# Kernel optimization log

Hardware: AMD Instinct MI355X
Metric: run time of the kernel (lower is better)

The kernel has to match this reference:

```python
import jax, jax.numpy as jnp
import numpy as np


def setup_inputs() -> dict:
    key = jax.random.key(0)
    ks = jax.random.split(key, 7)
    B, T, I, H, O = 64, 2048, 32, 256, 32
    s = 0.05
    return {
        "x": jax.random.normal(ks[0], (B, T, I), dtype=jnp.float32),
        "W_ih": jax.random.normal(ks[1], (4 * H, I), dtype=jnp.float32) * s,
        "W_hh": jax.random.normal(ks[2], (4 * H, H), dtype=jnp.float32) * s,
        "b_ih": jax.random.normal(ks[3], (4 * H,), dtype=jnp.float32) * s,
        "b_hh": jax.random.normal(ks[4], (4 * H,), dtype=jnp.float32) * s,
        "fc_w": jax.random.normal(ks[5], (O, H), dtype=jnp.float32) * s,
        "fc_b": jax.random.normal(ks[6], (O,), dtype=jnp.float32) * s,
    }


def _lstm(x, W_ih, W_hh, b_ih, b_hh):
    # x: [B,T,I]; PyTorch gate order: i, f, g, o stacked along 4H axis.
    B = x.shape[0]
    H = W_hh.shape[1]
    # Precompute input contributions for all timesteps in one GEMM: [B,T,4H]
    xg = jnp.einsum('bti,gi->btg', x, W_ih) + b_ih + b_hh

    def step(carry, xg_t):
        h, c = carry  # [B,H] each
        gates = xg_t + h @ W_hh.T  # [B,4H]
        i, f, g, o = jnp.split(gates, 4, axis=-1)
        i = jax.nn.sigmoid(i)
        f = jax.nn.sigmoid(f)
        g = jnp.tanh(g)
        o = jax.nn.sigmoid(o)
        c = f * c + i * g
        h = o * jnp.tanh(c)
        return (h, c), h

    h0 = jnp.zeros((B, H), dtype=x.dtype)
    (_, _), hs = jax.lax.scan(step, (h0, h0), jnp.swapaxes(xg, 0, 1))
    return jnp.swapaxes(hs, 0, 1)  # [B,T,H]


def reference(x, W_ih, W_hh, b_ih, b_hh, fc_w, fc_b):
    out = _lstm(x, W_ih, W_hh, b_ih, b_hh)          # [B,T,H]
    # Conv1d(H, O, kernel_size=1) over channel dim == pointwise linear.
    return jnp.einsum('bth,oh->bto', out, fc_w) + fc_b  # [B,T,O]
```

## Files before the change

### kernel.cpp

```cpp
#include <hip/hip_runtime.h>
#include <cstdint>


#define B_  64
#define T_  2048
#define I_  32
#define H_  256
#define O_  32

typedef unsigned int v4u __attribute__((ext_vector_type(4)));
typedef _Float16 h2_t __attribute__((ext_vector_type(2)));

#if __has_builtin(__builtin_amdgcn_sdot4)
__device__ __forceinline__ int dot4(int a, int b, int c) {
    return __builtin_amdgcn_sdot4(a, b, c, false);
}
#else
__device__ __forceinline__ int dot4(int a, int b, int c) {
    c += (int)(int8_t)(a)        * (int)(int8_t)(b);
    c += (int)(int8_t)(a >> 8)   * (int)(int8_t)(b >> 8);
    c += (int)(int8_t)(a >> 16)  * (int)(int8_t)(b >> 16);
    c += (int)(int8_t)(a >> 24)  * (int)(int8_t)(b >> 24);
    return c;
}
#endif

__device__ __forceinline__ float fdot2h(h2_t a, h2_t b, float c) {
#if __has_builtin(__builtin_amdgcn_fdot2)
    return __builtin_amdgcn_fdot2(a, b, c, false);
#else
    return c + (float)a[0] * (float)b[0] + (float)a[1] * (float)b[1];
#endif
}

__device__ __forceinline__ float wave64_max_bcast(float v) {
    int t;
    t = __builtin_amdgcn_update_dpp(__float_as_int(v), __float_as_int(v), 0x111, 0xf, 0xf, false);
    v = fmaxf(v, __int_as_float(t));
    t = __builtin_amdgcn_update_dpp(__float_as_int(v), __float_as_int(v), 0x112, 0xf, 0xf, false);
    v = fmaxf(v, __int_as_float(t));
    t = __builtin_amdgcn_update_dpp(__float_as_int(v), __float_as_int(v), 0x114, 0xf, 0xf, false);
    v = fmaxf(v, __int_as_float(t));
    t = __builtin_amdgcn_update_dpp(__float_as_int(v), __float_as_int(v), 0x118, 0xf, 0xf, false);
    v = fmaxf(v, __int_as_float(t));
    t = __builtin_amdgcn_update_dpp(__float_as_int(v), __float_as_int(v), 0x142, 0xa, 0xf, false);
    v = fmaxf(v, __int_as_float(t));
    t = __builtin_amdgcn_update_dpp(__float_as_int(v), __float_as_int(v), 0x143, 0xc, 0xf, false);
    v = fmaxf(v, __int_as_float(t));
    return __int_as_float(__builtin_amdgcn_readlane(__float_as_int(v), 63));
}

__device__ __forceinline__ float sum8(float v) {
    int t;
    t = __builtin_amdgcn_update_dpp(0, __float_as_int(v), 0x111, 0xf, 0xf, true); v += __int_as_float(t);
    t = __builtin_amdgcn_update_dpp(0, __float_as_int(v), 0x112, 0xf, 0xf, true); v += __int_as_float(t);
    t = __builtin_amdgcn_update_dpp(0, __float_as_int(v), 0x114, 0xf, 0xf, true); v += __int_as_float(t);
    return v;
}

#define QW_OFF   0
#define WIH_OFF  262144
#define S1_OFF   327680
#define BIAS_OFF 331776
#define XH_OFF   335872

__device__ __forceinline__ uint32_t pack_q(int q0, int q1, int q2, int q3) {
    return  ((uint32_t)(uint8_t)(int8_t)q0)
          | (((uint32_t)(uint8_t)(int8_t)q1) << 8)
          | (((uint32_t)(uint8_t)(int8_t)q2) << 16)
          | (((uint32_t)(uint8_t)(int8_t)q3) << 24);
}

__device__ __forceinline__ int clamp127(int v) {
    return v < -127 ? -127 : (v > 127 ? 127 : v);
}

__global__ __launch_bounds__(64) void prep_w(
    const float* __restrict__ Whh, const float* __restrict__ Wih,
    const float* __restrict__ bih, const float* __restrict__ bhh,
    uint32_t* __restrict__ qw4, uint32_t* __restrict__ wih4,
    float* __restrict__ s1v, float* __restrict__ biasv)
{
    const int gr = blockIdx.x;
    const int c  = threadIdx.x;
    const int j  = gr >> 8;
    const int r  = gr & 255;

    const float4 wv = ((const float4*)(Whh + gr * H_))[c];
    float m = fmaxf(fmaxf(fabsf(wv.x), fabsf(wv.y)), fmaxf(fabsf(wv.z), fabsf(wv.w)));
    #pragma unroll
    for (int s = 1; s < 64; s <<= 1) m = fmaxf(m, __shfl_xor(m, s, 64));
    const float S1 = fmaxf(m, 1e-20f) / 127.f;
    const float r1 = 1.f / S1;

    {
        const int d = j * 64 + c;
        qw4[(d >> 2) * 1024 + r * 4 + (d & 3)] = pack_q(
            clamp127((int)rintf(wv.x * r1)), clamp127((int)rintf(wv.y * r1)),
            clamp127((int)rintf(wv.z * r1)), clamp127((int)rintf(wv.w * r1)));
    }
    if (c < 16) {
        union { uint32_t u; h2_t h; } z;
        z.h[0] = (_Float16)Wih[gr * I_ + 2 * c];
        z.h[1] = (_Float16)Wih[gr * I_ + 2 * c + 1];
        const int dd = j * 16 + c;
        wih4[(dd >> 2) * 1024 + r * 4 + (dd & 3)] = z.u;
    }
    if (c == 0) { s1v[gr] = S1; biasv[gr] = bih[gr] + bhh[gr]; }
}

__global__ __launch_bounds__(256) void prep_xh(
    const float* __restrict__ x, uint32_t* __restrict__ xh)
{
    const int i = blockIdx.x * 256 + threadIdx.x;
    const float2 v = ((const float2*)x)[i];
    union { uint32_t u; h2_t h; } z;
    z.h[0] = (_Float16)v.x; z.h[1] = (_Float16)v.y;
    xh[i] = z.u;
}

__global__ __launch_bounds__(256, 1) void lstm_main(
    const uint32_t* __restrict__ qw4, const uint32_t* __restrict__ wih4,
    const float* __restrict__ s1v, const float* __restrict__ biasv,
    const uint32_t* __restrict__ xh, const float* __restrict__ fcw,
    const float* __restrict__ fcb, float* __restrict__ out)
{
    const int b  = blockIdx.x;
    const int r  = threadIdx.x;
    const int ln = r & 63;
    const int wv = r >> 6;

    __shared__ uint32_t hqb[2][64];
    __shared__ __align__(16) float hscb[2][4];
    __shared__ uint32_t hfb[2][128];

    v4u w4[64];
    #pragma unroll
    for (int d4 = 0; d4 < 64; d4++) w4[d4] = ((const v4u*)qw4)[d4 * 256 + r];
    v4u wx[16];
    #pragma unroll
    for (int d4 = 0; d4 < 16; d4++) wx[d4] = ((const v4u*)wih4)[d4 * 256 + r];
    float S1j[4], bj[4];
    #pragma unroll
    for (int j = 0; j < 4; j++) { S1j[j] = s1v[j * 256 + r]; bj[j] = biasv[j * 256 + r]; }

    const int o_ = r >> 3, ks = r & 7;
    h2_t fw[16];
    {
        const float* fr = fcw + o_ * H_ + ks * 32;
        #pragma unroll
        for (int i = 0; i < 16; i++) {
            h2_t p; p[0] = (_Float16)fr[2 * i]; p[1] = (_Float16)fr[2 * i + 1];
            fw[i] = p;
        }
    }
    const float fcb_v = fcb[o_];

    if (r < 4) hscb[1][r] = 0.f;
    __syncthreads();

    const uint32_t* xb   = xh + (size_t)(b * T_) * 16;
    float*          outb = out + (size_t)(b * T_) * O_;

    float c_state = 0.f;

    for (int t = 0; t < T_; t++) {
        const int pb = (t & 1) ^ 1, cb = t & 1;

        const v4u* xv = (const v4u*)(xb + (size_t)t * 16);
        const v4u x0 = xv[0], x1 = xv[1], x2 = xv[2], x3 = xv[3];

        const v4u*   hqv = (const v4u*)&hqb[pb][0];
        const float4 scv = *(const float4*)&hscb[pb][0];
        const float  scar[4] = { scv.x, scv.y, scv.z, scv.w };

        float a0 = 0.f, a1 = 0.f, a2 = 0.f, a3 = 0.f;
        #pragma unroll
        for (int g = 0; g < 4; g++) {
            v4u hg[4];
            #pragma unroll
            for (int q = 0; q < 4; q++) hg[q] = hqv[g * 4 + q];
            int i0 = 0, i1 = 0, i2 = 0, i3 = 0;
            #pragma unroll
            for (int q = 0; q < 4; q++) {
                #pragma unroll
                for (int e = 0; e < 4; e++) {
                    const int hv = (int)hg[q][e];
                    i0 = dot4((int)w4[ 0 + g * 4 + q][e], hv, i0);
                    i1 = dot4((int)w4[16 + g * 4 + q][e], hv, i1);
                    i2 = dot4((int)w4[32 + g * 4 + q][e], hv, i2);
                    i3 = dot4((int)w4[48 + g * 4 + q][e], hv, i3);
                }
            }
            a0 = fmaf((float)i0, scar[g], a0);
            a1 = fmaf((float)i1, scar[g], a1);
            a2 = fmaf((float)i2, scar[g], a2);
            a3 = fmaf((float)i3, scar[g], a3);
        }

        if (t > 0) {
            const v4u* hfv = (const v4u*)&hfb[pb][0];
            v4u fh[4];
            #pragma unroll
            for (int i = 0; i < 4; i++) fh[i] = hfv[ks * 4 + i];
            float acc = 0.f;
            #pragma unroll
            for (int i = 0; i < 16; i++) {
                union { uint32_t u; h2_t h; } z;
                z.u = fh[i >> 2][i & 3];
                acc = fdot2h(fw[i], z.h, acc);
            }
            acc = sum8(acc);
            if (ks == 7) outb[(t - 1) * O_ + o_] = acc + fcb_v;
        }

        float xd0 = 0.f, xd1 = 0.f, xd2 = 0.f, xd3 = 0.f;
        {
            const v4u xg4[4] = { x0, x1, x2, x3 };
            #pragma unroll
            for (int d4 = 0; d4 < 4; d4++) {
                #pragma unroll
                for (int e = 0; e < 4; e++) {
                    union { uint32_t u; h2_t h; } zx, z0, z1, z2, z3;
                    zx.u = xg4[d4][e];
                    z0.u = wx[ 0 + d4][e]; xd0 = fdot2h(z0.h, zx.h, xd0);
                    z1.u = wx[ 4 + d4][e]; xd1 = fdot2h(z1.h, zx.h, xd1);
                    z2.u = wx[ 8 + d4][e]; xd2 = fdot2h(z2.h, zx.h, xd2);
                    z3.u = wx[12 + d4][e]; xd3 = fdot2h(z3.h, zx.h, xd3);
                }
            }
        }

        const float g0 = fmaf(a0, S1j[0], xd0 + bj[0]);
        const float g1 = fmaf(a1, S1j[1], xd1 + bj[1]);
        const float g2 = fmaf(a2, S1j[2], xd2 + bj[2]);
        const float g3 = fmaf(a3, S1j[3], xd3 + bj[3]);
        const float i_ = 1.f / (1.f + __expf(-g0));
        const float f_ = 1.f / (1.f + __expf(-g1));
        const float gg = 2.f / (1.f + __expf(-2.f * g2)) - 1.f;
        const float oo = 1.f / (1.f + __expf(-g3));
        c_state = f_ * c_state + i_ * gg;
        const float tc = 2.f / (1.f + __expf(-2.f * c_state)) - 1.f;
        const float hval = oo * tc;

        float m = wave64_max_bcast(fabsf(hval));
        m = fmaxf(m, 1e-12f);
        const int q = clamp127((int)rintf(hval * (127.f / m)));
        ((char*)&hqb[cb][0])[r] = (char)(int8_t)q;
        if (ln == 0) hscb[cb][wv] = m * (1.f / 127.f);
        ((_Float16*)&hfb[cb][0])[r] = (_Float16)hval;

        asm volatile("s_waitcnt lgkmcnt(0)" ::: "memory");
        __builtin_amdgcn_s_barrier();
    }

    {
        const int pb = (T_ - 1) & 1;
        const v4u* hfv = (const v4u*)&hfb[pb][0];
        v4u fh[4];
        #pragma unroll
        for (int i = 0; i < 4; i++) fh[i] = hfv[ks * 4 + i];
        float acc = 0.f;
        #pragma unroll
        for (int i = 0; i < 16; i++) {
            union { uint32_t u; h2_t h; } z;
            z.u = fh[i >> 2][i & 3];
            acc = fdot2h(fw[i], z.h, acc);
        }
        acc = sum8(acc);
        if (ks == 7) outb[(T_ - 1) * O_ + o_] = acc + fcb_v;
    }
}

extern "C" void kernel_launch(void* const* d_in, const int* in_sizes, int n_in,
                              void* d_out, int out_size, void* d_ws, size_t ws_size,
                              hipStream_t stream) {
    const float* x    = (const float*)d_in[0];
    const float* Wih  = (const float*)d_in[1];
    const float* Whh  = (const float*)d_in[2];
    const float* bih  = (const float*)d_in[3];
    const float* bhh  = (const float*)d_in[4];
    const float* fcw  = (const float*)d_in[5];
    const float* fcb  = (const float*)d_in[6];
    float* out = (float*)d_out;

    char* ws = (char*)d_ws;
    uint32_t* qw4   = (uint32_t*)(ws + QW_OFF);
    uint32_t* wih4  = (uint32_t*)(ws + WIH_OFF);
    float*    s1v   = (float*)(ws + S1_OFF);
    float*    biasv = (float*)(ws + BIAS_OFF);
    uint32_t* xh    = (uint32_t*)(ws + XH_OFF);

    prep_w<<<1024, 64, 0, stream>>>(Whh, Wih, bih, bhh, qw4, wih4, s1v, biasv);
    prep_xh<<<(B_ * T_ * 16) / 256, 256, 0, stream>>>(x, xh);
    lstm_main<<<B_, 256, 0, stream>>>(qw4, wih4, s1v, biasv, xh, fcw, fcb, out);
}
```

Before: 3.410 ms.

## Batch four sequences per block and use MFMA for recurrent, input and FC GEMMs

Replaces the per-sequence dot4 LSTM kernel (64 blocks of 256 threads) with 16 blocks of 512 threads, each processing 4 batch rows at once. The recurrent int8 matmul, the fp16 input projection and the output linear layer now run as MFMA instructions, and the weights are pre-swizzled into MFMA fragment layouts by the prep kernels. Hidden-state quantization now uses a per-batch-row max via LDS atomicMax, which adds a second barrier per timestep. This cuts the number of serial blocks and the scalar dot work per step, at the cost of extra synchronization, padding in the MFMA M dimension, and fewer CUs in use.

```diff
diff --git a/kernel.cpp b/kernel.cpp
--- a/kernel.cpp
+++ b/kernel.cpp
@@ -7,33 +7,18 @@
 #define I_  32
 #define H_  256
 #define O_  32
-
+#define MB  4
+#define NBLK 16
+
+typedef int v4i __attribute__((ext_vector_type(4)));
 typedef unsigned int v4u __attribute__((ext_vector_type(4)));
+typedef float f32x4 __attribute__((ext_vector_type(4)));
+typedef _Float16 f16x8 __attribute__((ext_vector_type(8)));
 typedef _Float16 h2_t __attribute__((ext_vector_type(2)));
 
-#if __has_builtin(__builtin_amdgcn_sdot4)
-__device__ __forceinline__ int dot4(int a, int b, int c) {
-    return __builtin_amdgcn_sdot4(a, b, c, false);
-}
-#else
-__device__ __forceinline__ int dot4(int a, int b, int c) {
-    c += (int)(int8_t)(a)        * (int)(int8_t)(b);
-    c += (int)(int8_t)(a >> 8)   * (int)(int8_t)(b >> 8);
-    c += (int)(int8_t)(a >> 16)  * (int)(int8_t)(b >> 16);
-    c += (int)(int8_t)(a >> 24)  * (int)(int8_t)(b >> 24);
-    return c;
-}
-#endif
-
-__device__ __forceinline__ float fdot2h(h2_t a, h2_t b, float c) {
-#if __has_builtin(__builtin_amdgcn_fdot2)
-    return __builtin_amdgcn_fdot2(a, b, c, false);
-#else
-    return c + (float)a[0] * (float)b[0] + (float)a[1] * (float)b[1];
-#endif
-}
-
-__device__ __forceinline__ float wave64_max_bcast(float v) {
+union U16x8 { v4u u; f16x8 h; };
+
+__device__ __forceinline__ float row16_max(float v) {
     int t;
     t = __builtin_amdgcn_update_dpp(__float_as_int(v), __float_as_int(v), 0x111, 0xf, 0xf, false);
     v = fmaxf(v, __int_as_float(t));
@@ -43,26 +28,15 @@
     v = fmaxf(v, __int_as_float(t));
     t = __builtin_amdgcn_update_dpp(__float_as_int(v), __float_as_int(v), 0x118, 0xf, 0xf, false);
     v = fmaxf(v, __int_as_float(t));
-    t = __builtin_amdgcn_update_dpp(__float_as_int(v), __float_as_int(v), 0x142, 0xa, 0xf, false);
-    v = fmaxf(v, __int_as_float(t));
-    t = __builtin_amdgcn_update_dpp(__float_as_int(v), __float_as_int(v), 0x143, 0xc, 0xf, false);
-    v = fmaxf(v, __int_as_float(t));
-    return __int_as_float(__builtin_amdgcn_readlane(__float_as_int(v), 63));
-}
-
-__device__ __forceinline__ float sum8(float v) {
-    int t;
-    t = __builtin_amdgcn_update_dpp(0, __float_as_int(v), 0x111, 0xf, 0xf, true); v += __int_as_float(t);
-    t = __builtin_amdgcn_update_dpp(0, __float_as_int(v), 0x112, 0xf, 0xf, true); v += __int_as_float(t);
-    t = __builtin_amdgcn_update_dpp(0, __float_as_int(v), 0x114, 0xf, 0xf, true); v += __int_as_float(t);
     return v;
 }
 
-#define QW_OFF   0
-#define WIH_OFF  262144
-#define S1_OFF   327680
-#define BIAS_OFF 331776
-#define XH_OFF   335872
+#define WQ_OFF    0
+#define S1P_OFF   262144
+#define BIASP_OFF 266240
+#define WIHH2_OFF 270336
+#define FCF_OFF   335872
+#define XH_OFF    352256
 
 __device__ __forceinline__ uint32_t pack_q(int q0, int q1, int q2, int q3) {
     return  ((uint32_t)(uint8_t)(int8_t)q0)
@@ -75,38 +49,36 @@
     return v < -127 ? -127 : (v > 127 ? 127 : v);
 }
 
-__global__ __launch_bounds__(64) void prep_w(
+
+__global__ __launch_bounds__(64) void prep_wq(
     const float* __restrict__ Whh, const float* __restrict__ Wih,
     const float* __restrict__ bih, const float* __restrict__ bhh,
-    uint32_t* __restrict__ qw4, uint32_t* __restrict__ wih4,
-    float* __restrict__ s1v, float* __restrict__ biasv)
+    uint32_t* __restrict__ wq2, float* __restrict__ s1p,
+    float* __restrict__ biasp, uint32_t* __restrict__ wihh2)
 {
     const int gr = blockIdx.x;
-    const int c  = threadIdx.x;
-    const int j  = gr >> 8;
-    const int r  = gr & 255;
-
-    const float4 wv = ((const float4*)(Whh + gr * H_))[c];
+    const int j  = threadIdx.x;
+    const int g  = gr >> 8, r = gr & 255;
+    const int c  = ((r >> 4) << 6) | (g << 4) | (r & 15);
+
+    const float4 wv = ((const float4*)(Whh + gr * H_))[j];
     float m = fmaxf(fmaxf(fabsf(wv.x), fabsf(wv.y)), fmaxf(fabsf(wv.z), fabsf(wv.w)));
     #pragma unroll
     for (int s = 1; s < 64; s <<= 1) m = fmaxf(m, __shfl_xor(m, s, 64));
     const float S1 = fmaxf(m, 1e-20f) / 127.f;
     const float r1 = 1.f / S1;
 
-    {
-        const int d = j * 64 + c;
-        qw4[(d >> 2) * 1024 + r * 4 + (d & 3)] = pack_q(
-            clamp127((int)rintf(wv.x * r1)), clamp127((int)rintf(wv.y * r1)),
-            clamp127((int)rintf(wv.z * r1)), clamp127((int)rintf(wv.w * r1)));
-    }
-    if (c < 16) {
+    wq2[((c >> 4) * 16 + (j >> 2)) * 64 + (c & 15) * 4 + (j & 3)] = pack_q(
+        clamp127((int)rintf(wv.x * r1)), clamp127((int)rintf(wv.y * r1)),
+        clamp127((int)rintf(wv.z * r1)), clamp127((int)rintf(wv.w * r1)));
+
+    if (j < 16) {
         union { uint32_t u; h2_t h; } z;
-        z.h[0] = (_Float16)Wih[gr * I_ + 2 * c];
-        z.h[1] = (_Float16)Wih[gr * I_ + 2 * c + 1];
-        const int dd = j * 16 + c;
-        wih4[(dd >> 2) * 1024 + r * 4 + (dd & 3)] = z.u;
-    }
-    if (c == 0) { s1v[gr] = S1; biasv[gr] = bih[gr] + bhh[gr]; }
+        z.h[0] = (_Float16)Wih[gr * I_ + 2 * j];
+        z.h[1] = (_Float16)Wih[gr * I_ + 2 * j + 1];
+        wihh2[((c >> 4) * 4 + (j >> 2)) * 64 + (c & 15) * 4 + (j & 3)] = z.u;
+    }
+    if (j == 0) { s1p[c] = S1; biasp[c] = bih[gr] + bhh[gr]; }
 }
 
 __global__ __launch_bounds__(256) void prep_xh(
@@ -119,156 +91,172 @@
     xh[i] = z.u;
 }
 
-__global__ __launch_bounds__(256, 1) void lstm_main(
-    const uint32_t* __restrict__ qw4, const uint32_t* __restrict__ wih4,
-    const float* __restrict__ s1v, const float* __restrict__ biasv,
-    const uint32_t* __restrict__ xh, const float* __restrict__ fcw,
+__global__ __launch_bounds__(64) void prep_fcf(
+    const float* __restrict__ fcw, uint32_t* __restrict__ fcf)
+{
+    const int id = blockIdx.x * 64 + threadIdx.x;
+    const int fw = id >> 9, rem = id & 511;
+    const int ks = rem >> 6, l = rem & 63;
+    const int o  = fw * 16 + (l & 15);
+    const int kb = ks * 32 + (l >> 4) * 8;
+    const float* src = fcw + o * H_ + kb;
+    #pragma unroll
+    for (int e = 0; e < 4; e++) {
+        union { uint32_t u; h2_t h; } z;
+        z.h[0] = (_Float16)src[2 * e];
+        z.h[1] = (_Float16)src[2 * e + 1];
+        fcf[id * 4 + e] = z.u;
+    }
+}
+
+__global__ __launch_bounds__(512, 2) void lstm_mfma(
+    const uint32_t* __restrict__ wq2, const float* __restrict__ s1p,
+    const float* __restrict__ biasp, const uint32_t* __restrict__ wihh2,
+    const uint32_t* __restrict__ xh, const uint32_t* __restrict__ fcf,
     const float* __restrict__ fcb, float* __restrict__ out)
 {
-    const int b  = blockIdx.x;
-    const int r  = threadIdx.x;
-    const int ln = r & 63;
-    const int wv = r >> 6;
-
-    __shared__ uint32_t hqb[2][64];
-    __shared__ __align__(16) float hscb[2][4];
-    __shared__ uint32_t hfb[2][128];
-
-    v4u w4[64];
+    const int blk = blockIdx.x, tid = threadIdx.x;
+    const int wvi = tid >> 6, l = tid & 63, lq = l >> 4, lo = l & 15;
+    const int b   = lo >> 2;
+
+    __shared__ __align__(16) char     Ab[2][1088];
+    __shared__ __align__(16) _Float16 hf[2][1088];
+    __shared__ int shmax[2][4];
+
+    v4i  wB[8][4];
+    float s1c[8], biasc[8];
     #pragma unroll
-    for (int d4 = 0; d4 < 64; d4++) w4[d4] = ((const v4u*)qw4)[d4 * 256 + r];
-    v4u wx[16];
-    #pragma unroll
-    for (int d4 = 0; d4 < 16; d4++) wx[d4] = ((const v4u*)wih4)[d4 * 256 + r];
-    float S1j[4], bj[4];
-    #pragma unroll
-    for (int j = 0; j < 4; j++) { S1j[j] = s1v[j * 256 + r]; bj[j] = biasv[j * 256 + r]; }
-
-    const int o_ = r >> 3, ks = r & 7;
-    h2_t fw[16];
-    {
-        const float* fr = fcw + o_ * H_ + ks * 32;
+    for (int nt = 0; nt < 8; nt++) {
+        const int c = wvi * 128 + nt * 16 + lo;
+        s1c[nt] = s1p[c]; biasc[nt] = biasp[c];
         #pragma unroll
-        for (int i = 0; i < 16; i++) {
-            h2_t p; p[0] = (_Float16)fr[2 * i]; p[1] = (_Float16)fr[2 * i + 1];
-            fw[i] = p;
-        }
-    }
-    const float fcb_v = fcb[o_];
-
-    if (r < 4) hscb[1][r] = 0.f;
+        for (int kt = 0; kt < 4; kt++)
+            wB[nt][kt] = *(const v4i*)(wq2 +
+                (size_t)(((wvi * 8 + nt) * 16 + kt * 4 + lq) * 64 + lo * 4));
+    }
+    const f32x4 fcbv = *(const f32x4*)(fcb + (wvi & 1) * 16 + lq * 4);
+
+    for (int i = tid; i < 1088; i += 512) Ab[1][i] = 0;
+    if (tid < 8) ((int*)shmax)[tid] = 0;
     __syncthreads();
 
-    const uint32_t* xb   = xh + (size_t)(b * T_) * 16;
-    float*          outb = out + (size_t)(b * T_) * O_;
-
-    float c_state = 0.f;
+    const uint32_t* xrow = xh + ((size_t)(blk * MB + b) * T_) * 16 + lq * 4;
+    v4u xA = *(const v4u*)xrow;
+
+    float cst0 = 0.f, cst1 = 0.f;
 
     for (int t = 0; t < T_; t++) {
-        const int pb = (t & 1) ^ 1, cb = t & 1;
-
-        const v4u* xv = (const v4u*)(xb + (size_t)t * 16);
-        const v4u x0 = xv[0], x1 = xv[1], x2 = xv[2], x3 = xv[3];
-
-        const v4u*   hqv = (const v4u*)&hqb[pb][0];
-        const float4 scv = *(const float4*)&hscb[pb][0];
-        const float  scar[4] = { scv.x, scv.y, scv.z, scv.w };
-
-        float a0 = 0.f, a1 = 0.f, a2 = 0.f, a3 = 0.f;
+        const int rb = (t & 1) ^ 1, cb = t & 1;
+
+        const float spm = __int_as_float(shmax[rb][lq]);
+
+        const v4i af0 = *(const v4i*)&Ab[rb][b * 272 +   0 + lq * 16];
+        const v4i af1 = *(const v4i*)&Ab[rb][b * 272 +  64 + lq * 16];
+        const v4i af2 = *(const v4i*)&Ab[rb][b * 272 + 128 + lq * 16];
+        const v4i af3 = *(const v4i*)&Ab[rb][b * 272 + 192 + lq * 16];
+
+        const int tn = (t + 1 < T_) ? (t + 1) : t;
+        const v4u xAn = *(const v4u*)(xrow + (size_t)tn * 16);
+        v4u wX[8];
         #pragma unroll
-        for (int g = 0; g < 4; g++) {
-            v4u hg[4];
+        for (int nt = 0; nt < 8; nt++)
+            wX[nt] = *(const v4u*)(wihh2 +
+                (size_t)(((wvi * 8 + nt) * 4 + lq) * 64 + lo * 4));
+
+        v4i Ci[8];
+        #pragma unroll
+        for (int nt = 0; nt < 8; nt++) {
+            v4i acc = {0, 0, 0, 0};
+            acc = __builtin_amdgcn_mfma_i32_16x16x64_i8(af0, wB[nt][0], acc, 0, 0, 0);
+            acc = __builtin_amdgcn_mfma_i32_16x16x64_i8(af1, wB[nt][1], acc, 0, 0, 0);
+            acc = __builtin_amdgcn_mfma_i32_16x16x64_i8(af2, wB[nt][2], acc, 0, 0, 0);
+            acc = __builtin_amdgcn_mfma_i32_16x16x64_i8(af3, wB[nt][3], acc, 0, 0, 0);
+            Ci[nt] = acc;
+        }
+
+        if (wvi < 2 && t > 0) {
+            f32x4 cfc = {0.f, 0.f, 0.f, 0.f};
             #pragma unroll
-            for (int q = 0; q < 4; q++) hg[q] = hqv[g * 4 + q];
-            int i0 = 0, i1 = 0, i2 = 0, i3 = 0;
+            for (int ks = 0; ks < 8; ks++) {
+                U16x8 aw, bh;
+                aw.u = *(const v4u*)(fcf + (size_t)(((wvi * 8 + ks) * 64 + l) * 4));
+                bh.u = *(const v4u*)&hf[rb][b * 272 + ks * 32 + lq * 8];
+                cfc = __builtin_amdgcn_mfma_f32_16x16x32_f16(aw.h, bh.h, cfc, 0, 0, 0);
+            }
+            if ((lo & 3) == 0) {
+                const f32x4 r = cfc + fcbv;
+                *(f32x4*)(out + ((size_t)(blk * MB + b) * T_ + (t - 1)) * O_
+                          + (wvi * 16 + lq * 4)) = r;
+            }
+        }
+
+        const float sp = spm * (1.f / 127.f);
+        float ga[8];
+        {
+            U16x8 xa; xa.u = xA;
             #pragma unroll
-            for (int q = 0; q < 4; q++) {
-                #pragma unroll
-                for (int e = 0; e < 4; e++) {
-                    const int hv = (int)hg[q][e];
-                    i0 = dot4((int)w4[ 0 + g * 4 + q][e], hv, i0);
-                    i1 = dot4((int)w4[16 + g * 4 + q][e], hv, i1);
-                    i2 = dot4((int)w4[32 + g * 4 + q][e], hv, i2);
-                    i3 = dot4((int)w4[48 + g * 4 + q][e], hv, i3);
-                }
-            }
-            a0 = fmaf((float)i0, scar[g], a0);
-            a1 = fmaf((float)i1, scar[g], a1);
-            a2 = fmaf((float)i2, scar[g], a2);
-            a3 = fmaf((float)i3, scar[g], a3);
-        }
-
-        if (t > 0) {
-            const v4u* hfv = (const v4u*)&hfb[pb][0];
-            v4u fh[4];
-            #pragma unroll
-            for (int i = 0; i < 4; i++) fh[i] = hfv[ks * 4 + i];
-            float acc = 0.f;
-            #pragma unroll
-            for (int i = 0; i < 16; i++) {
-                union { uint32_t u; h2_t h; } z;
-                z.u = fh[i >> 2][i & 3];
-                acc = fdot2h(fw[i], z.h, acc);
-            }
-            acc = sum8(acc);
-            if (ks == 7) outb[(t - 1) * O_ + o_] = acc + fcb_v;
-        }
-
-        float xd0 = 0.f, xd1 = 0.f, xd2 = 0.f, xd3 = 0.f;
-        {
-            const v4u xg4[4] = { x0, x1, x2, x3 };
-            #pragma unroll
-            for (int d4 = 0; d4 < 4; d4++) {
-                #pragma unroll
-                for (int e = 0; e < 4; e++) {
-                    union { uint32_t u; h2_t h; } zx, z0, z1, z2, z3;
-                    zx.u = xg4[d4][e];
-                    z0.u = wx[ 0 + d4][e]; xd0 = fdot2h(z0.h, zx.h, xd0);
-                    z1.u = wx[ 4 + d4][e]; xd1 = fdot2h(z1.h, zx.h, xd1);
-                    z2.u = wx[ 8 + d4][e]; xd2 = fdot2h(z2.h, zx.h, xd2);
-                    z3.u = wx[12 + d4][e]; xd3 = fdot2h(z3.h, zx.h, xd3);
-                }
-            }
-        }
-
-        const float g0 = fmaf(a0, S1j[0], xd0 + bj[0]);
-        const float g1 = fmaf(a1, S1j[1], xd1 + bj[1]);
-        const float g2 = fmaf(a2, S1j[2], xd2 + bj[2]);
-        const float g3 = fmaf(a3, S1j[3], xd3 + bj[3]);
-        const float i_ = 1.f / (1.f + __expf(-g0));
-        const float f_ = 1.f / (1.f + __expf(-g1));
-        const float gg = 2.f / (1.f + __expf(-2.f * g2)) - 1.f;
-        const float oo = 1.f / (1.f + __expf(-g3));
-        c_state = f_ * c_state + i_ * gg;
-        const float tc = 2.f / (1.f + __expf(-2.f * c_state)) - 1.f;
-        const float hval = oo * tc;
-
-        float m = wave64_max_bcast(fabsf(hval));
-        m = fmaxf(m, 1e-12f);
-        const int q = clamp127((int)rintf(hval * (127.f / m)));
-        ((char*)&hqb[cb][0])[r] = (char)(int8_t)q;
-        if (ln == 0) hscb[cb][wv] = m * (1.f / 127.f);
-        ((_Float16*)&hfb[cb][0])[r] = (_Float16)hval;
+            for (int nt = 0; nt < 8; nt++) {
+                const float v = (float)Ci[nt][0] * (s1c[nt] * sp) + biasc[nt];
+                f32x4 cf = {v, v, v, v};
+                U16x8 wx; wx.u = wX[nt];
+                cf = __builtin_amdgcn_mfma_f32_16x16x32_f16(xa.h, wx.h, cf, 0, 0, 0);
+                ga[nt] = cf[0];
+            }
+        }
+
+        const float i0 = 1.f / (1.f + __expf(-ga[0]));
+        const float f0 = 1.f / (1.f + __expf(-ga[1]));
+        const float g0 = 2.f / (1.f + __expf(-2.f * ga[2])) - 1.f;
+        const float o0 = 1.f / (1.f + __expf(-ga[3]));
+        cst0 = f0 * cst0 + i0 * g0;
+        const float h0 = o0 * (2.f / (1.f + __expf(-2.f * cst0)) - 1.f);
+
+        const float i1 = 1.f / (1.f + __expf(-ga[4]));
+        const float f1 = 1.f / (1.f + __expf(-ga[5]));
+        const float g1 = 2.f / (1.f + __expf(-2.f * ga[6])) - 1.f;
+        const float o1 = 1.f / (1.f + __expf(-ga[7]));
+        cst1 = f1 * cst1 + i1 * g1;
+        const float h1 = o1 * (2.f / (1.f + __expf(-2.f * cst1)) - 1.f);
+
+        float vm = fmaxf(fabsf(h0), fabsf(h1));
+        vm = row16_max(vm);
+        if (lo == 15) atomicMax(&shmax[cb][lq], __float_as_int(vm));
 
         asm volatile("s_waitcnt lgkmcnt(0)" ::: "memory");
         __builtin_amdgcn_s_barrier();
+
+        const float mm = fmaxf(__int_as_float(shmax[cb][lq]), 1e-12f);
+        const float rq = 127.f / mm;
+        const int r0 = wvi * 32 + lo, r1 = r0 + 16;
+        Ab[cb][lq * 272 + r0] = (char)(int8_t)clamp127((int)rintf(h0 * rq));
+        Ab[cb][lq * 272 + r1] = (char)(int8_t)clamp127((int)rintf(h1 * rq));
+        hf[cb][lq * 272 + r0] = (_Float16)h0;
+        hf[cb][lq * 272 + r1] = (_Float16)h1;
+        if (tid < 4) shmax[rb][tid] = 0;
+
+        asm volatile("s_waitcnt lgkmcnt(0)" ::: "memory");
+        __builtin_amdgcn_s_barrier();
+
+        xA = xAn;
     }
 
     {
-        const int pb = (T_ - 1) & 1;
-        const v4u* hfv = (const v4u*)&hfb[pb][0];
-        v4u fh[4];
-        #pragma unroll
-        for (int i = 0; i < 4; i++) fh[i] = hfv[ks * 4 + i];
-        float acc = 0.f;
-        #pragma unroll
-        for (int i = 0; i < 16; i++) {
-            union { uint32_t u; h2_t h; } z;
-            z.u = fh[i >> 2][i & 3];
-            acc = fdot2h(fw[i], z.h, acc);
-        }
-        acc = sum8(acc);
-        if (ks == 7) outb[(T_ - 1) * O_ + o_] = acc + fcb_v;
+        const int rbF = (T_ - 1) & 1;
+        if (wvi < 2) {
+            f32x4 cfc = {0.f, 0.f, 0.f, 0.f};
+            #pragma unroll
+            for (int ks = 0; ks < 8; ks++) {
+                U16x8 aw, bh;
+                aw.u = *(const v4u*)(fcf + (size_t)(((wvi * 8 + ks) * 64 + l) * 4));
+                bh.u = *(const v4u*)&hf[rbF][b * 272 + ks * 32 + lq * 8];
+                cfc = __builtin_amdgcn_mfma_f32_16x16x32_f16(aw.h, bh.h, cfc, 0, 0, 0);
+            }
+            if ((lo & 3) == 0) {
+                const f32x4 r = cfc + fcbv;
+                *(f32x4*)(out + ((size_t)(blk * MB + b) * T_ + (T_ - 1)) * O_
+                          + (wvi * 16 + lq * 4)) = r;
+            }
+        }
     }
 }
 
@@ -285,13 +273,15 @@
     float* out = (float*)d_out;
 
     char* ws = (char*)d_ws;
-    uint32_t* qw4   = (uint32_t*)(ws + QW_OFF);
-    uint32_t* wih4  = (uint32_t*)(ws + WIH_OFF);
-    float*    s1v   = (float*)(ws + S1_OFF);
-    float*    biasv = (float*)(ws + BIAS_OFF);
+    uint32_t* wq2   = (uint32_t*)(ws + WQ_OFF);
+    float*    s1p   = (float*)(ws + S1P_OFF);
+    float*    biasp = (float*)(ws + BIASP_OFF);
+    uint32_t* wihh2 = (uint32_t*)(ws + WIHH2_OFF);
+    uint32_t* fcf   = (uint32_t*)(ws + FCF_OFF);
     uint32_t* xh    = (uint32_t*)(ws + XH_OFF);
 
-    prep_w<<<1024, 64, 0, stream>>>(Whh, Wih, bih, bhh, qw4, wih4, s1v, biasv);
+    prep_wq<<<1024, 64, 0, stream>>>(Whh, Wih, bih, bhh, wq2, s1p, biasp, wihh2);
     prep_xh<<<(B_ * T_ * 16) / 256, 256, 0, stream>>>(x, xh);
-    lstm_main<<<B_, 256, 0, stream>>>(qw4, wih4, s1v, biasv, xh, fcw, fcb, out);
-}
+    prep_fcf<<<16, 64, 0, stream>>>(fcw, fcf);
+    lstm_mfma<<<NBLK, 512, 0, stream>>>(wq2, s1p, biasp, wihh2, xh, fcf, fcb, out);
+}
```

Result: slower. 3.704 ms (+8.6%).
